# Optimization experiments

Hardware: AMD Instinct MI355X
Metric: run time of the kernel (lower is better)

## Reference

```python
import jax, jax.numpy as jnp
import numpy as np

B, L, D = 8, 2048, 256
D_MODEL = 1024
NUM_SIGNALS = 16
MAX_POSITIONS = 4096
ROLE_OUTPUT = 2  # role id used for the CLS token


def setup_inputs() -> dict:
    key = jax.random.key(0)
    ks = jax.random.split(key, 12)
    emb = jax.random.normal(ks[0], (B, L, D), dtype=jnp.float32)
    pos = jax.random.randint(ks[1], (B, L), 1, MAX_POSITIONS + 1)          # pos >= 1 for real tokens
    sid = jax.random.randint(ks[2], (B, L), 0, NUM_SIGNALS)
    role = jax.random.randint(ks[3], (B, L), 0, 3)
    padding_mask = jax.random.uniform(ks[4], (B, L)) < 0.75                # True = real token
    # learned parameters
    proj_W = jax.random.normal(ks[5], (NUM_SIGNALS, D_MODEL, D), dtype=jnp.float32) * (1.0 / np.sqrt(D))
    proj_b = jax.random.normal(ks[6], (NUM_SIGNALS, D_MODEL), dtype=jnp.float32) * 0.01
    cls_content = jax.random.normal(ks[7], (D_MODEL,), dtype=jnp.float32)
    pos_embed = jax.random.normal(ks[8], (MAX_POSITIONS + 1, D_MODEL), dtype=jnp.float32)
    id_embed = jax.random.normal(ks[9], (NUM_SIGNALS + 1, D_MODEL), dtype=jnp.float32)
    role_embed = jax.random.normal(ks[10], (3, D_MODEL), dtype=jnp.float32)
    return dict(emb=emb, pos=pos, sid=sid, role=role, padding_mask=padding_mask,
                proj_W=proj_W, proj_b=proj_b, cls_content=cls_content,
                pos_embed=pos_embed, id_embed=id_embed, role_embed=role_embed)


def reference(emb, pos, sid, role, padding_mask,
              proj_W, proj_b, cls_content, pos_embed, id_embed, role_embed):
    Bv, Lv, _ = emb.shape
    S, d_model, _ = proj_W.shape
    cls_id = S

    # Grouped per-signal projection: one GEMM per signal id, select per token.
    tokens = jnp.zeros((Bv, Lv, d_model), dtype=emb.dtype)
    for s in range(S):
        proj_s = jnp.einsum('bld,ed->ble', emb, proj_W[s]) + proj_b[s]   # (B, L, d_model)
        keep = ((sid == s) & padding_mask)[..., None]
        tokens = jnp.where(keep, proj_s, tokens)

    # Prepend CLS
    cls = jnp.broadcast_to(cls_content[None, None, :], (Bv, 1, d_model))
    tokens = jnp.concatenate([cls, tokens], axis=1)                       # (B, L+1, d_model)

    pos_full = jnp.concatenate([jnp.zeros((Bv, 1), dtype=pos.dtype), pos], axis=1)
    sid_full = jnp.concatenate([jnp.full((Bv, 1), cls_id, dtype=sid.dtype), sid], axis=1)
    role_full = jnp.concatenate([jnp.full((Bv, 1), ROLE_OUTPUT, dtype=role.dtype), role], axis=1)

    tokens = tokens + pos_embed[pos_full] + id_embed[sid_full] + role_embed[role_full]

    attn_keep = jnp.concatenate([jnp.ones((Bv, 1), dtype=bool), padding_mask], axis=1)
    return tokens, attn_keep
```

## Files before the change

kernel.cpp:

```cpp
#include <hip/hip_runtime.h>
#include <hip/hip_bf16.h>
#include <stdint.h>

#define B_ 8
#define L_ 2048
#define NTOK 16384
#define DK 256
#define DM 1024
#define NS 16
#define LOUT 2049
#define TOK_OUT (B_*LOUT*DM)
#define ATTN_OUT (B_*LOUT)
#define PCAP 2048
#define UCAP 8192

typedef unsigned short u16;
typedef unsigned int u32;
typedef __bf16 bf16x8 __attribute__((ext_vector_type(8)));
typedef float f32x4 __attribute__((ext_vector_type(4)));

__device__ inline u32 packbf2(float lo, float hi) {
    u32 a, b;
    __builtin_memcpy(&a, &lo, 4);
    __builtin_memcpy(&b, &hi, 4);
    a = (a + 0x8000u) >> 16;
    b = (b + 0x8000u) & 0xFFFF0000u;
    return a | b;
}

__device__ inline void gll16(const void* g, void* l) {
    __builtin_amdgcn_global_load_lds(
        (const __attribute__((address_space(1))) unsigned int*)g,
        (__attribute__((address_space(3))) unsigned int*)l, 16, 0, 0);
}

#define WS_CUR 0
#define WS_UCUR 16
#define WS_WIDTH 32
#define WS_PERM 64
#define WS_UNM (64 + NS * PCAP)
#define EMB_OFF 262144ULL
#define W_OFF (EMB_OFF + 16384ULL * 512ULL)
#define WS_NEED (W_OFF + 16384ULL * 512ULL)

__device__ inline int sniff_width(const unsigned char* mb, int tid, int* sh) {
    if (tid == 0) { sh[0] = 0; sh[1] = 0; sh[2] = 0; }
    __syncthreads();
    int c1ge2 = 0, ge2 = 0, oddnz = 0;
    const u32* mw = (const u32*)mb;
    #pragma unroll
    for (int i = 0; i < 16; i++) {
        u32 x = mw[tid * 16 + i];
        u32 b0 = x & 0xFF, b1 = (x >> 8) & 0xFF, b2 = (x >> 16) & 0xFF, b3 = x >> 24;
        if (b1 >= 2) c1ge2 = 1;
        if (b0 >= 2 || b1 >= 2 || b2 >= 2 || b3 >= 2) ge2 = 1;
        if ((b1 | b3) != 0) oddnz = 1;
    }
    if (c1ge2) atomicOr(&sh[0], 1);
    if (ge2) atomicOr(&sh[1], 1);
    if (oddnz) atomicOr(&sh[2], 1);
    __syncthreads();
    if (sh[0]) return 2;
    if (sh[1]) return 4;
    if (sh[2]) return 1;
    return 4;
}

__device__ inline int decode_mask(const unsigned char* mb, int t, int width) {
    if (width == 1) return mb[t] != 0;
    if (width == 2) return ((const u16*)mb)[t] != 0;
    return ((const u32*)mb)[t] != 0;
}

#define SORT_B 64
#define PREP_GRID (SORT_B + 1024)

__global__ __launch_bounds__(256) void prep_all(
    const unsigned char* __restrict__ mb, const int* __restrict__ sid,
    const float* __restrict__ emb, const float* __restrict__ W,
    int* __restrict__ wsi, unsigned char* __restrict__ wsb) {
    __shared__ int sh[3];
    __shared__ int lcnt[NS], gbase[NS];
    __shared__ int lcnt_u, gbase_u;
    int bid = blockIdx.x;
    int tid = threadIdx.x;
    int lane = tid & 63;
    int wv = tid >> 6;

    if (bid < SORT_B) {
        if (tid < NS) lcnt[tid] = 0;
        if (tid == 0) lcnt_u = 0;
        int width = sniff_width(mb, tid, sh);
        if (bid == 0 && tid == 0) wsi[WS_WIDTH] = width;
        int t = bid * 256 + tid;
        int m = decode_mask(mb, t, width);
        int s = sid[t];
        int lr;
        if (m) lr = atomicAdd(&lcnt[s], 1);
        else   lr = atomicAdd(&lcnt_u, 1);
        __syncthreads();
        if (tid < NS) gbase[tid] = atomicAdd(&wsi[WS_CUR + tid], lcnt[tid]);
        if (tid == 0) gbase_u = atomicAdd(&wsi[WS_UCUR], lcnt_u);
        __syncthreads();
        if (m) {
            int r = gbase[s] + lr;
            if (r < PCAP) wsi[WS_PERM + s * PCAP + r] = t;
        } else {
            int r = gbase_u + lr;
            if (r < UCAP) wsi[WS_UNM + r] = t;
        }
        return;
    }

    int cb = bid - SORT_B;
    const float* src;
    u16* dst;
    if (cb < 512) {
        src = emb;
        dst = (u16*)(wsb + EMB_OFF);
    } else {
        cb -= 512;
        src = W;
        dst = (u16*)(wsb + W_OFF);
    }
    int r0 = cb * 32 + wv * 8;
    #pragma unroll 4
    for (int i = 0; i < 8; i++) {
        int r = r0 + i;
        float4 a = *(const float4*)(src + (size_t)r * DK + lane * 4);
        uint2 o;
        o.x = packbf2(a.x, a.y);
        o.y = packbf2(a.z, a.w);
        *(uint2*)(dst + (size_t)r * DK + lane * 4) = o;
    }
}

#define GG 1280
#define CLS_B0 (GG - 67)
#define ATTN_B0 (GG - 65)

__global__ __launch_bounds__(256, 4) void gemm_big(
    const unsigned char* __restrict__ mb,
    const int* __restrict__ pos, const int* __restrict__ sid,
    const int* __restrict__ role,
    const float* __restrict__ bias, const float* __restrict__ cls,
    const float* __restrict__ pos_emb, const float* __restrict__ id_emb,
    const float* __restrict__ role_emb,
    const int* __restrict__ wsi, const unsigned char* __restrict__ wsb,
    float* __restrict__ out) {
    __shared__ u16 As[2][128 * 32];
    __shared__ u16 Bs[2][128 * 32];
    __shared__ int toks[128];
    int bi = (int)blockIdx.x;
    int tid = threadIdx.x;
    int lane = tid & 63;
    int wv = tid >> 6;

    int cnts[NS];
    int mtot = 0;
    #pragma unroll
    for (int i = 0; i < NS; i++) {
        int c = wsi[WS_CUR + i];
        cnts[i] = c > PCAP ? PCAP : c;
        mtot += (cnts[i] + 127) >> 7;
    }
    int xcd = bi & 7;
    int j = bi >> 3;
    int m_lo = (xcd * mtot) >> 3;
    int m_hi = ((xcd + 1) * mtot) >> 3;
    int cm = m_hi - m_lo;
    bool doGemm = (cm > 0 && j < cm * 8);
    int s = -1, lrt = 0, n0 = 0;
    if (doGemm) {
        int nt = j & 7;
        int m = m_lo + (j >> 3);
        n0 = nt << 7;
        #pragma unroll
        for (int i = 0; i < NS; i++) {
            int rt = (cnts[i] + 127) >> 7;
            if (s < 0) {
                if (m < rt) { s = i; lrt = m; }
                else m -= rt;
            }
        }
        if (s < 0) doGemm = false;
    }

    if (doGemm) {
        int rowsValid = cnts[s] - lrt * 128;
        if (rowsValid > 128) rowsValid = 128;

        if (tid < 128) {
            int base = WS_PERM + s * PCAP + lrt * 128;
            toks[tid] = wsi[base + ((tid < rowsValid) ? tid : 0)];
        }
        __syncthreads();

        const u16* Eb = (const u16*)(wsb + EMB_OFF);
        const u16* Bb = (const u16*)(wsb + W_OFF) + (size_t)(s * DM + n0) * DK;

        int srow = lane >> 2;
        int slseg = lane & 3;
        int arow = wv * 16 + srow;
        int ags = (slseg - (arow >> 1)) & 3;
        const u16* AsrcLo = Eb + (size_t)toks[arow] * DK;
        const u16* AsrcHi = Eb + (size_t)toks[arow + 64] * DK;

        f32x4 acc[4][4];
        #pragma unroll
        for (int im = 0; im < 4; im++)
            #pragma unroll
            for (int jn = 0; jn < 4; jn++) acc[im][jn] = (f32x4){0.f, 0.f, 0.f, 0.f};

        int wm = wv & 1, wn = wv >> 1;
        int mcol = lane & 15;
        int quad = lane >> 4;

#define STAGE(kc, bf)                                                          \
        {                                                                      \
            gll16(AsrcLo + (kc) * 32 + ags * 8, &As[bf][(wv * 16) * 32]);      \
            gll16(AsrcHi + (kc) * 32 + ags * 8, &As[bf][(64 + wv * 16) * 32]); \
            gll16(Bb + (size_t)arow * DK + (kc) * 32 + ags * 8,                \
                  &Bs[bf][(wv * 16) * 32]);                                    \
            gll16(Bb + (size_t)(64 + arow) * DK + (kc) * 32 + ags * 8,         \
                  &Bs[bf][(64 + wv * 16) * 32]);                               \
        }

        STAGE(0, 0)
        #pragma unroll
        for (int kc = 0; kc < 8; ++kc) {
            __syncthreads();
            if (kc < 7) STAGE(kc + 1, (kc + 1) & 1)
            int bf = kc & 1;
            bf16x8 af[4], bfr[4];
            #pragma unroll
            for (int im = 0; im < 4; im++) {
                int row = wm * 64 + im * 16 + mcol;
                int sg = (quad + (row >> 1)) & 3;
                af[im] = *(const bf16x8*)(&As[bf][row * 32 + sg * 8]);
            }
            #pragma unroll
            for (int jn = 0; jn < 4; jn++) {
                int row = wn * 64 + jn * 16 + mcol;
                int sg = (quad + (row >> 1)) & 3;
                bfr[jn] = *(const bf16x8*)(&Bs[bf][row * 32 + sg * 8]);
            }
            #pragma unroll
            for (int im = 0; im < 4; im++)
                #pragma unroll
                for (int jn = 0; jn < 4; jn++)
                    acc[im][jn] = __builtin_amdgcn_mfma_f32_16x16x32_bf16(
                        af[im], bfr[jn], acc[im][jn], 0, 0, 0);
        }
#undef STAGE

        float bc[4];
        #pragma unroll
        for (int jn = 0; jn < 4; jn++) {
            int col = n0 + wn * 64 + jn * 16 + mcol;
            bc[jn] = bias[s * DM + col] + id_emb[s * DM + col];
        }
        #pragma unroll
        for (int im = 0; im < 4; im++) {
            #pragma unroll
            for (int r = 0; r < 4; r++) {
                int rowT = wm * 64 + im * 16 + quad * 4 + r;
                if (rowT >= rowsValid) continue;
                int t = toks[rowT];
                int p = pos[t];
                int ro = role[t];
                int b = t >> 11, l = t & 2047;
                size_t orow = (size_t)(b * LOUT + l + 1) * DM;
                const float* prow = pos_emb + (size_t)p * DM;
                const float* rrow = role_emb + (size_t)ro * DM;
                float pv[4], rv[4];
                #pragma unroll
                for (int jn = 0; jn < 4; jn++) {
                    int col = n0 + wn * 64 + jn * 16 + mcol;
                    pv[jn] = prow[col];
                    rv[jn] = rrow[col];
                }
                #pragma unroll
                for (int jn = 0; jn < 4; jn++) {
                    int col = n0 + wn * 64 + jn * 16 + mcol;
                    float val = acc[im][jn][r] + bc[jn] + pv[jn] + rv[jn];
                    __builtin_nontemporal_store(val, &out[orow + col]);
                }
            }
        }
    }

    {
        int ucnt = wsi[WS_UCUR];
        if (ucnt > UCAP) ucnt = UCAP;
        for (int idx = (GG - 1 - bi) * 4 + wv; idx < ucnt; idx += GG * 4) {
            int t = wsi[WS_UNM + idx];
            int p = pos[t], sd = sid[t], ro = role[t];
            int b = t >> 11, l = t & 2047;
            size_t orow = (size_t)(b * LOUT + l + 1) * DM;
            const float* pr = pos_emb + (size_t)p * DM;
            const float* ir = id_emb + (size_t)sd * DM;
            const float* rr = role_emb + (size_t)ro * DM;
            #pragma unroll
            for (int it = 0; it < 4; it++) {
                int c = it * 256 + lane * 4;
                f32x4 a = *(const f32x4*)(pr + c);
                f32x4 d = *(const f32x4*)(ir + c);
                f32x4 e = *(const f32x4*)(rr + c);
                f32x4 o = a + d + e;
                __builtin_nontemporal_store(o, (f32x4*)(out + orow + c));
            }
        }
        if (bi >= CLS_B0 && bi < ATTN_B0) {
            int b = (bi - CLS_B0) * 4 + wv;
            size_t orow = (size_t)(b * LOUT) * DM;
            #pragma unroll
            for (int it = 0; it < 4; it++) {
                int c = it * 256 + lane * 4;
                f32x4 cc = *(const f32x4*)(cls + c);
                f32x4 a = *(const f32x4*)(pos_emb + c);
                f32x4 d = *(const f32x4*)(id_emb + NS * DM + c);
                f32x4 e = *(const f32x4*)(role_emb + 2 * DM + c);
                f32x4 o = cc + a + d + e;
                *(f32x4*)(out + orow + c) = o;
            }
        }
        if (bi >= ATTN_B0) {
            int width = wsi[WS_WIDTH];
            int i = (bi - ATTN_B0) * 256 + tid;
            if (i < ATTN_OUT) {
                int b = i / LOUT;
                int jj = i - b * LOUT;
                float val = (jj == 0) ? 1.0f
                    : (float)decode_mask(mb, b * L_ + jj - 1, width);
                out[TOK_OUT + i] = val;
            }
        }
    }
}

extern "C" void kernel_launch(void* const* d_in, const int* in_sizes, int n_in,
                              void* d_out, int out_size, void* d_ws, size_t ws_size,
                              hipStream_t stream) {
    const float* emb = (const float*)d_in[0];
    const int* pos = (const int*)d_in[1];
    const int* sid = (const int*)d_in[2];
    const int* role = (const int*)d_in[3];
    const unsigned char* mask = (const unsigned char*)d_in[4];
    const float* W = (const float*)d_in[5];
    const float* bias = (const float*)d_in[6];
    const float* cls = (const float*)d_in[7];
    const float* pos_emb = (const float*)d_in[8];
    const float* id_emb = (const float*)d_in[9];
    const float* role_emb = (const float*)d_in[10];
    float* out = (float*)d_out;
    int* wsi = (int*)d_ws;
    unsigned char* wsb = (unsigned char*)d_ws;

    (void)hipMemsetAsync(wsi, 0, 64 * sizeof(int), stream);
    hipLaunchKernelGGL(prep_all, dim3(PREP_GRID), dim3(256), 0, stream,
                       mask, sid, emb, W, wsi, wsb);
    hipLaunchKernelGGL(gemm_big, dim3(GG), dim3(256), 0, stream,
                       mask, pos, sid, role, bias, cls, pos_emb, id_emb,
                       role_emb, wsi, wsb, out);
}
```

Baseline: 154.5 us.

## Fuse prep and GEMM kernels into one cooperative persistent kernel with grid sync

Merges the sort/convert prep kernel and the grouped GEMM kernel into a single cooperative launch of 1024 blocks. The blocks loop over the prep work, do a grid-wide sync, then loop over the GEMM tiles. The aim is to remove the second kernel launch and the gap between the two kernels. The cost is that grid-sync overhead, a fixed grid of 1024 blocks and strided virtual-block loops may unbalance the GEMM tiles. If the cooperative launch fails, it falls back to the original two kernels.

```diff
diff --git a/kernel.cpp b/kernel.cpp
--- a/kernel.cpp
+++ b/kernel.cpp
@@ -1,6 +1,9 @@
 #include <hip/hip_runtime.h>
 #include <hip/hip_bf16.h>
+#include <hip/hip_cooperative_groups.h>
 #include <stdint.h>
+
+namespace cg = cooperative_groups;
 
 #define B_ 8
 #define L_ 2048
@@ -42,6 +45,12 @@
 #define EMB_OFF 262144ULL
 #define W_OFF (EMB_OFF + 16384ULL * 512ULL)
 #define WS_NEED (W_OFF + 16384ULL * 512ULL)
+
+__device__ inline int decode_mask(const unsigned char* mb, int t, int width) {
+    if (width == 1) return mb[t] != 0;
+    if (width == 2) return ((const u16*)mb)[t] != 0;
+    return ((const u32*)mb)[t] != 0;
+}
 
 __device__ inline int sniff_width(const unsigned char* mb, int tid, int* sh) {
     if (tid == 0) { sh[0] = 0; sh[1] = 0; sh[2] = 0; }
@@ -66,53 +75,37 @@
     return 4;
 }
 
-__device__ inline int decode_mask(const unsigned char* mb, int t, int width) {
-    if (width == 1) return mb[t] != 0;
-    if (width == 2) return ((const u16*)mb)[t] != 0;
-    return ((const u32*)mb)[t] != 0;
-}
-
-#define SORT_B 64
-#define PREP_GRID (SORT_B + 1024)
-
-__global__ __launch_bounds__(256) void prep_all(
-    const unsigned char* __restrict__ mb, const int* __restrict__ sid,
-    const float* __restrict__ emb, const float* __restrict__ W,
-    int* __restrict__ wsi, unsigned char* __restrict__ wsb) {
-    __shared__ int sh[3];
-    __shared__ int lcnt[NS], gbase[NS];
-    __shared__ int lcnt_u, gbase_u;
-    int bid = blockIdx.x;
-    int tid = threadIdx.x;
-    int lane = tid & 63;
-    int wv = tid >> 6;
-
-    if (bid < SORT_B) {
-        if (tid < NS) lcnt[tid] = 0;
-        if (tid == 0) lcnt_u = 0;
-        int width = sniff_width(mb, tid, sh);
-        if (bid == 0 && tid == 0) wsi[WS_WIDTH] = width;
-        int t = bid * 256 + tid;
-        int m = decode_mask(mb, t, width);
-        int s = sid[t];
-        int lr;
-        if (m) lr = atomicAdd(&lcnt[s], 1);
-        else   lr = atomicAdd(&lcnt_u, 1);
-        __syncthreads();
-        if (tid < NS) gbase[tid] = atomicAdd(&wsi[WS_CUR + tid], lcnt[tid]);
-        if (tid == 0) gbase_u = atomicAdd(&wsi[WS_UCUR], lcnt_u);
-        __syncthreads();
-        if (m) {
-            int r = gbase[s] + lr;
-            if (r < PCAP) wsi[WS_PERM + s * PCAP + r] = t;
-        } else {
-            int r = gbase_u + lr;
-            if (r < UCAP) wsi[WS_UNM + r] = t;
-        }
-        return;
-    }
-
-    int cb = bid - SORT_B;
+struct SortSh { int sh[3]; int lcnt[NS]; int gbase[NS]; int lcnt_u; int gbase_u; };
+
+__device__ inline void sort_body(int bid, int tid, SortSh& S,
+                                 const unsigned char* mb, const int* sid,
+                                 int* wsi) {
+    if (tid < NS) S.lcnt[tid] = 0;
+    if (tid == 0) S.lcnt_u = 0;
+    int width = sniff_width(mb, tid, S.sh);
+    if (bid == 0 && tid == 0) wsi[WS_WIDTH] = width;
+    int t = bid * 256 + tid;
+    int m = decode_mask(mb, t, width);
+    int s = sid[t];
+    int lr;
+    if (m) lr = atomicAdd(&S.lcnt[s], 1);
+    else   lr = atomicAdd(&S.lcnt_u, 1);
+    __syncthreads();
+    if (tid < NS) S.gbase[tid] = atomicAdd(&wsi[WS_CUR + tid], S.lcnt[tid]);
+    if (tid == 0) S.gbase_u = atomicAdd(&wsi[WS_UCUR], S.lcnt_u);
+    __syncthreads();
+    if (m) {
+        int r = S.gbase[s] + lr;
+        if (r < PCAP) wsi[WS_PERM + s * PCAP + r] = t;
+    } else {
+        int r = S.gbase_u + lr;
+        if (r < UCAP) wsi[WS_UNM + r] = t;
+    }
+}
+
+__device__ inline void conv_body(int cb, int lane, int wv,
+                                 const float* emb, const float* W,
+                                 unsigned char* wsb) {
     const float* src;
     u16* dst;
     if (cb < 512) {
@@ -139,23 +132,14 @@
 #define CLS_B0 (GG - 67)
 #define ATTN_B0 (GG - 65)
 
-__global__ __launch_bounds__(256, 4) void gemm_big(
-    const unsigned char* __restrict__ mb,
-    const int* __restrict__ pos, const int* __restrict__ sid,
-    const int* __restrict__ role,
-    const float* __restrict__ bias, const float* __restrict__ cls,
-    const float* __restrict__ pos_emb, const float* __restrict__ id_emb,
-    const float* __restrict__ role_emb,
-    const int* __restrict__ wsi, const unsigned char* __restrict__ wsb,
-    float* __restrict__ out) {
-    __shared__ u16 As[2][128 * 32];
-    __shared__ u16 Bs[2][128 * 32];
-    __shared__ int toks[128];
-    int bi = (int)blockIdx.x;
-    int tid = threadIdx.x;
-    int lane = tid & 63;
-    int wv = tid >> 6;
-
+__device__ inline void gemm_body(
+    int bi, int tid, int lane, int wv,
+    u16 (*As)[128 * 32], u16 (*Bs)[128 * 32], int* toks,
+    const unsigned char* mb,
+    const int* pos, const int* sid, const int* role,
+    const float* bias, const float* cls,
+    const float* pos_emb, const float* id_emb, const float* role_emb,
+    const int* wsi, const unsigned char* wsb, float* out) {
     int cnts[NS];
     int mtot = 0;
     #pragma unroll
@@ -339,14 +323,81 @@
     }
 }
 
+#define CGRID 1024
+#define PREP_V 1088
+
+__global__ __launch_bounds__(256, 4) void mega(
+    const unsigned char* __restrict__ mb,
+    const int* __restrict__ pos, const int* __restrict__ sid,
+    const int* __restrict__ role,
+    const float* __restrict__ emb, const float* __restrict__ W,
+    const float* __restrict__ bias, const float* __restrict__ cls,
+    const float* __restrict__ pos_emb, const float* __restrict__ id_emb,
+    const float* __restrict__ role_emb,
+    int* __restrict__ wsi, unsigned char* __restrict__ wsb,
+    float* __restrict__ out) {
+    __shared__ u16 As[2][128 * 32];
+    __shared__ u16 Bs[2][128 * 32];
+    __shared__ int toks[128];
+    __shared__ SortSh S;
+    int bi0 = (int)blockIdx.x;
+    int tid = threadIdx.x;
+    int lane = tid & 63;
+    int wv = tid >> 6;
+
+    for (int v = bi0; v < PREP_V; v += CGRID) {
+        if (v < 64) sort_body(v, tid, S, mb, sid, wsi);
+        else conv_body(v - 64, lane, wv, emb, W, wsb);
+    }
+    cg::this_grid().sync();
+
+    for (int v = bi0; v < GG; v += CGRID) {
+        __syncthreads();
+        gemm_body(v, tid, lane, wv, As, Bs, toks, mb, pos, sid, role,
+                  bias, cls, pos_emb, id_emb, role_emb, wsi, wsb, out);
+    }
+}
+
+#define SORT_B 64
+#define PREP_GRID (SORT_B + 1024)
+
+__global__ __launch_bounds__(256) void prep_all(
+    const unsigned char* __restrict__ mb, const int* __restrict__ sid,
+    const float* __restrict__ emb, const float* __restrict__ W,
+    int* __restrict__ wsi, unsigned char* __restrict__ wsb) {
+    __shared__ SortSh S;
+    int bid = blockIdx.x;
+    int tid = threadIdx.x;
+    if (bid < SORT_B) sort_body(bid, tid, S, mb, sid, wsi);
+    else conv_body(bid - SORT_B, tid & 63, tid >> 6, emb, W, wsb);
+}
+
+__global__ __launch_bounds__(256, 4) void gemm_big(
+    const unsigned char* __restrict__ mb,
+    const int* __restrict__ pos, const int* __restrict__ sid,
+    const int* __restrict__ role,
+    const float* __restrict__ bias, const float* __restrict__ cls,
+    const float* __restrict__ pos_emb, const float* __restrict__ id_emb,
+    const float* __restrict__ role_emb,
+    const int* __restrict__ wsi, const unsigned char* __restrict__ wsb,
+    float* __restrict__ out) {
+    __shared__ u16 As[2][128 * 32];
+    __shared__ u16 Bs[2][128 * 32];
+    __shared__ int toks[128];
+    int tid = threadIdx.x;
+    gemm_body((int)blockIdx.x, tid, tid & 63, tid >> 6, As, Bs, toks,
+              mb, pos, sid, role, bias, cls, pos_emb, id_emb, role_emb,
+              wsi, wsb, out);
+}
+
 extern "C" void kernel_launch(void* const* d_in, const int* in_sizes, int n_in,
                               void* d_out, int out_size, void* d_ws, size_t ws_size,
                               hipStream_t stream) {
-    const float* emb = (const float*)d_in[0];
+    const unsigned char* mask = (const unsigned char*)d_in[4];
     const int* pos = (const int*)d_in[1];
     const int* sid = (const int*)d_in[2];
     const int* role = (const int*)d_in[3];
-    const unsigned char* mask = (const unsigned char*)d_in[4];
+    const float* emb = (const float*)d_in[0];
     const float* W = (const float*)d_in[5];
     const float* bias = (const float*)d_in[6];
     const float* cls = (const float*)d_in[7];
@@ -358,9 +409,18 @@
     unsigned char* wsb = (unsigned char*)d_ws;
 
     (void)hipMemsetAsync(wsi, 0, 64 * sizeof(int), stream);
-    hipLaunchKernelGGL(prep_all, dim3(PREP_GRID), dim3(256), 0, stream,
-                       mask, sid, emb, W, wsi, wsb);
-    hipLaunchKernelGGL(gemm_big, dim3(GG), dim3(256), 0, stream,
-                       mask, pos, sid, role, bias, cls, pos_emb, id_emb,
-                       role_emb, wsi, wsb, out);
-}
+
+    void* args[] = {(void*)&mask, (void*)&pos, (void*)&sid, (void*)&role,
+                    (void*)&emb, (void*)&W, (void*)&bias, (void*)&cls,
+                    (void*)&pos_emb, (void*)&id_emb, (void*)&role_emb,
+                    (void*)&wsi, (void*)&wsb, (void*)&out};
+    hipError_t err = hipLaunchCooperativeKernel(
+        (const void*)mega, dim3(CGRID), dim3(256), args, 0, stream);
+    if (err != hipSuccess) {
+        hipLaunchKernelGGL(prep_all, dim3(PREP_GRID), dim3(256), 0, stream,
+                           mask, sid, emb, W, wsi, wsb);
+        hipLaunchKernelGGL(gemm_big, dim3(GG), dim3(256), 0, stream,
+                           mask, pos, sid, role, bias, cls, pos_emb, id_emb,
+                           role_emb, wsi, wsb, out);
+    }
+}
```

New measurement: 355.8 us. +130.4%, slower.
